# Kernel optimization log

Hardware: AMD Instinct MI355X
Metric: run time of the kernel (lower is better)

The kernel has to match this reference:

```python
import jax, jax.numpy as jnp
import numpy as np

V, D, L, H, DH, F, T, NL = 65536, 1024, 12, 16, 64, 3584, 2048, 2


def _ln(x, w, b):
    m = x.mean(-1, keepdims=True)
    v = ((x - m) ** 2).mean(-1, keepdims=True)
    return (x - m) * jax.lax.rsqrt(v + 1e-5) * w + b


def setup_inputs() -> dict:
    key = jax.random.key(0)
    ks = iter(jax.random.split(key, 64))
    nrm = lambda shape, s=0.02: jax.random.normal(next(ks), shape, jnp.float32) * s
    uni = lambda shape: jax.random.uniform(next(ks), shape, jnp.float32)
    inp = {
        'idx': jax.random.randint(next(ks), (T,), 0, V),
        'emb': nrm((V, D)),
        'ln0_w': jnp.ones((D,), jnp.float32), 'ln0_b': jnp.zeros((D,), jnp.float32),
        'ln1_w': jnp.ones((L, D), jnp.float32), 'ln1_b': jnp.zeros((L, D), jnp.float32),
        'mix_r': uni((L, D)), 'mix_k': uni((L, D)), 'mix_v': uni((L, D)), 'mix_g': uni((L, D)),
        'decay': nrm((L, H, DH), 0.5),  # w = exp(-exp(decay))
        'faaaa': nrm((L, H, DH), 0.1),  # per-head bonus u
        'Wr': nrm((L, D, D)), 'Wk': nrm((L, D, D)), 'Wv': nrm((L, D, D)),
        'Wg': nrm((L, D, D)), 'Wo': nrm((L, D, D)),
        'lnx_w': jnp.ones((L, D), jnp.float32), 'lnx_b': jnp.zeros((L, D), jnp.float32),
        'ln2_w': jnp.ones((L, D), jnp.float32), 'ln2_b': jnp.zeros((L, D), jnp.float32),
        'cmix_k': uni((L, D)), 'cmix_r': uni((L, D)),
        'cWk': nrm((L, D, F)), 'cWv': nrm((L, F, D)), 'cWr': nrm((L, D, D)),
        'lnout_w': jnp.ones((D,), jnp.float32), 'lnout_b': jnp.zeros((D,), jnp.float32),
        'score_w': nrm((NL, D)),
    }
    return inp


def _forward(idx, emb, ln0_w, ln0_b, ln1_w, ln1_b, mix_r, mix_k, mix_v, mix_g,
             decay, faaaa, Wr, Wk, Wv, Wg, Wo, lnx_w, lnx_b, ln2_w, ln2_b,
             cmix_k, cmix_r, cWk, cWv, cWr, lnout_w, lnout_b, score_w):
    x = _ln(emb[idx], ln0_w, ln0_b)  # (T, D); RWKV ln0 on embeddings
    zrow = jnp.zeros((1, D), x.dtype)
    for i in range(L):
        # ---- time mixing (RWKV-5 WKV) ----
        xn = _ln(x, ln1_w[i], ln1_b[i])
        sx = jnp.concatenate([zrow, xn[:-1]], 0)  # token shift, zero init state
        xr = xn * mix_r[i] + sx * (1 - mix_r[i])
        xk = xn * mix_k[i] + sx * (1 - mix_k[i])
        xv = xn * mix_v[i] + sx * (1 - mix_v[i])
        xg = xn * mix_g[i] + sx * (1 - mix_g[i])
        r = (xr @ Wr[i]).reshape(T, H, DH)
        k = (xk @ Wk[i]).reshape(T, H, DH)
        v = (xv @ Wv[i]).reshape(T, H, DH)
        g = jax.nn.silu(xg @ Wg[i])  # (T, D)
        wdec = jnp.exp(-jnp.exp(decay[i]))  # (H, DH) per-channel decay
        uu = faaaa[i]                       # (H, DH) bonus
        def step(S, rkv, wdec=wdec, uu=uu):
            rt, kt, vt = rkv                      # each (H, DH)
            a = kt[:, :, None] * vt[:, None, :]   # (H, DH, DH) outer product
            o = jnp.einsum('hd,hde->he', rt, uu[:, :, None] * a + S)
            return wdec[:, :, None] * S + a, o
        S0 = jnp.zeros((H, DH, DH), x.dtype)
        _, wkv = jax.lax.scan(step, S0, (r, k, v))  # wkv: (T, H, DH)
        # per-head group norm, then affine over full D
        m = wkv.mean(-1, keepdims=True)
        var = ((wkv - m) ** 2).mean(-1, keepdims=True)
        gn = ((wkv - m) * jax.lax.rsqrt(var + 1e-5)).reshape(T, D) * lnx_w[i] + lnx_b[i]
        x = x + (gn * g) @ Wo[i]
        # ---- channel mixing ----
        xn2 = _ln(x, ln2_w[i], ln2_b[i])
        sx2 = jnp.concatenate([zrow, xn2[:-1]], 0)
        xk2 = xn2 * cmix_k[i] + sx2 * (1 - cmix_k[i])
        xr2 = xn2 * cmix_r[i] + sx2 * (1 - cmix_r[i])
        kk = jnp.square(jax.nn.relu(xk2 @ cWk[i]))  # (T, F)
        x = x + jax.nn.sigmoid(xr2 @ cWr[i]) * (kk @ cWv[i])
    x = _ln(x, lnout_w, lnout_b)
    logits = x @ score_w.T  # (T, NL)
    return logits[-1]       # pooled_logits


def reference(idx, emb, ln0_w, ln0_b, ln1_w, ln1_b, mix_r, mix_k, mix_v, mix_g,
              decay, faaaa, Wr, Wk, Wv, Wg, Wo, lnx_w, lnx_b, ln2_w, ln2_b,
              cmix_k, cmix_r, cWk, cWv, cWr, lnout_w, lnout_b, score_w):
    return _forward(idx, emb, ln0_w, ln0_b, ln1_w, ln1_b, mix_r, mix_k, mix_v, mix_g,
                    decay, faaaa, Wr, Wk, Wv, Wg, Wo, lnx_w, lnx_b, ln2_w, ln2_b,
                    cmix_k, cmix_r, cWk, cWv, cWr, lnout_w, lnout_b, score_w)
```

## Files before the change

### kernel.cpp

```cpp
#include <hip/hip_runtime.h>
#include <stdint.h>
#include <math.h>

#define T_SEQ 2048
#define DIM   1024
#define NLAY  12
#define NH    16
#define DHH   64
#define FF    3584
#define CHUNK 32
#define NCH   64

typedef __bf16 bf16;
typedef __attribute__((ext_vector_type(8))) __bf16 bf16x8;
typedef __attribute__((ext_vector_type(4))) __bf16 bf16x4;
typedef __attribute__((ext_vector_type(4))) float f32x4;

#define AS1 __attribute__((address_space(1)))
#define AS3 __attribute__((address_space(3)))

__device__ __forceinline__ void async_cp16(const bf16* g, bf16* l) {
  __builtin_amdgcn_global_load_lds((AS1 void*)(uintptr_t)g, (AS3 void*)l, 16, 0, 0);
}

__device__ __forceinline__ float siluf(float x) { return x / (1.f + expf(-x)); }

__device__ __forceinline__ void block_reduce_4(float& a, float& b, float& c, float& d) {
#pragma unroll
  for (int off = 32; off >= 1; off >>= 1) {
    a += __shfl_xor(a, off, 64);
    b += __shfl_xor(b, off, 64);
    c += __shfl_xor(c, off, 64);
    d += __shfl_xor(d, off, 64);
  }
  __shared__ float red[4][4];
  int wid = threadIdx.x >> 6;
  if ((threadIdx.x & 63) == 0) { red[wid][0] = a; red[wid][1] = b; red[wid][2] = c; red[wid][3] = d; }
  __syncthreads();
  a = red[0][0] + red[1][0] + red[2][0] + red[3][0];
  b = red[0][1] + red[1][1] + red[2][1] + red[3][1];
  c = red[0][2] + red[1][2] + red[2][2] + red[3][2];
  d = red[0][3] + red[1][3] + red[2][3] + red[3][3];
}

__global__ __launch_bounds__(256) void k_embed(const int* __restrict__ idx,
                                               const float* __restrict__ emb,
                                               const float* __restrict__ w,
                                               const float* __restrict__ b,
                                               float* __restrict__ x) {
  int t = blockIdx.x, tid = threadIdx.x, c = tid * 4;
  long row = idx[t];
  float4 xc = *(const float4*)&emb[row * DIM + c];
  float s = xc.x + xc.y + xc.z + xc.w;
  float q = xc.x * xc.x + xc.y * xc.y + xc.z * xc.z + xc.w * xc.w;
  float d2 = 0.f, d3 = 0.f;
  block_reduce_4(s, q, d2, d3);
  float m = s * (1.f / DIM), var = q * (1.f / DIM) - m * m;
  float rs = rsqrtf(var + 1e-5f);
  float4 lw = *(const float4*)&w[c], lb = *(const float4*)&b[c];
  float4 o;
  o.x = (xc.x - m) * rs * lw.x + lb.x;
  o.y = (xc.y - m) * rs * lw.y + lb.y;
  o.z = (xc.z - m) * rs * lw.z + lb.z;
  o.w = (xc.w - m) * rs * lw.w + lb.w;
  *(float4*)&x[(long)t * DIM + c] = o;
}

__global__ __launch_bounds__(256) void k_lnmix(const float* __restrict__ x,
                                               const float* __restrict__ lnw,
                                               const float* __restrict__ lnb,
                                               const float* __restrict__ mx0,
                                               const float* __restrict__ mx1,
                                               const float* __restrict__ mx2,
                                               const float* __restrict__ mx3,
                                               bf16* __restrict__ out, int nmix) {
  int t = blockIdx.x, tid = threadIdx.x, c = tid * 4;
  float4 xc = *(const float4*)&x[(long)t * DIM + c];
  float4 xp = {0.f, 0.f, 0.f, 0.f};
  if (t > 0) xp = *(const float4*)&x[(long)(t - 1) * DIM + c];
  float s1 = xc.x + xc.y + xc.z + xc.w;
  float q1 = xc.x * xc.x + xc.y * xc.y + xc.z * xc.z + xc.w * xc.w;
  float s2 = xp.x + xp.y + xp.z + xp.w;
  float q2 = xp.x * xp.x + xp.y * xp.y + xp.z * xp.z + xp.w * xp.w;
  block_reduce_4(s1, q1, s2, q2);
  float m1 = s1 * (1.f / DIM), v1 = q1 * (1.f / DIM) - m1 * m1, rs1 = rsqrtf(v1 + 1e-5f);
  float m2 = s2 * (1.f / DIM), v2 = q2 * (1.f / DIM) - m2 * m2, rs2 = rsqrtf(v2 + 1e-5f);
  float4 lw = *(const float4*)&lnw[c], lb = *(const float4*)&lnb[c];
  float xs[4] = {xc.x, xc.y, xc.z, xc.w}, xps[4] = {xp.x, xp.y, xp.z, xp.w};
  float lws[4] = {lw.x, lw.y, lw.z, lw.w}, lbs[4] = {lb.x, lb.y, lb.z, lb.w};
  float xn[4], sx[4];
#pragma unroll
  for (int j = 0; j < 4; j++) {
    xn[j] = (xs[j] - m1) * rs1 * lws[j] + lbs[j];
    sx[j] = (t > 0) ? ((xps[j] - m2) * rs2 * lws[j] + lbs[j]) : 0.f;
  }
  for (int mi = 0; mi < nmix; mi++) {
    const float* mp = (mi == 0) ? mx0 : (mi == 1) ? mx1 : (mi == 2) ? mx2 : mx3;
    float4 mv = *(const float4*)&mp[c];
    float ms[4] = {mv.x, mv.y, mv.z, mv.w};
    bf16x4 o;
#pragma unroll
    for (int j = 0; j < 4; j++) o[j] = (bf16)(xn[j] * ms[j] + sx[j] * (1.f - ms[j]));
    *(bf16x4*)&out[(long)mi * T_SEQ * DIM + (long)t * DIM + c] = o;
  }
}

struct TrArgs {
  const float* src[8];
  bf16* dst[8];
  int K[8];
  int N[8];
  int tstart[9];
};

__global__ __launch_bounds__(256) void k_trans(TrArgs a) {
  int bid = blockIdx.x;
  int m = 0;
#pragma unroll
  for (int i = 1; i < 8; i++)
    if (bid >= a.tstart[i]) m = i;
  int tl = bid - a.tstart[m];
  int N = a.N[m], K = a.K[m];
  int ntN = N >> 6;
  int tn = tl % ntN, tk = tl / ntN;
  const float* src = a.src[m];
  bf16* dst = a.dst[m];
  __shared__ __align__(16) float tile[64][65];
  int tid = threadIdx.x;
  int r = tid >> 2, cq = (tid & 3) * 16;
  const float* sp = &src[(long)(tk * 64 + r) * N + tn * 64 + cq];
#pragma unroll
  for (int j = 0; j < 16; j += 4) {
    float4 v = *(const float4*)&sp[j];
    tile[r][cq + j] = v.x;
    tile[r][cq + j + 1] = v.y;
    tile[r][cq + j + 2] = v.z;
    tile[r][cq + j + 3] = v.w;
  }
  __syncthreads();
  int rn = tid >> 2, kq = (tid & 3) * 16;
  bf16* dp = &dst[(long)(tn * 64 + rn) * K + tk * 64 + kq];
#pragma unroll
  for (int h = 0; h < 2; h++) {
    bf16x8 o8;
#pragma unroll
    for (int j = 0; j < 8; j++) o8[j] = (bf16)tile[kq + h * 8 + j][rn];
    *(bf16x8*)&dp[h * 8] = o8;
  }
}

#define BMT 128
#define BKT 32

template <int MODE, int BN>
__global__ __launch_bounds__(256) void k_gemm(const bf16* __restrict__ A,
                                              const bf16* __restrict__ Bt,
                                              void* __restrict__ OUTv,
                                              const float* __restrict__ AUX,
                                              int M, int N, int K,
                                              long zsA, long zsB, long zsO) {
  constexpr int NJ = BN / 32;
  __shared__ __align__(16) bf16 sA[2][BMT * BKT];
  __shared__ __align__(16) bf16 sB[2][BN * BKT];
  int z = blockIdx.z;
  A += (long)z * zsA;
  Bt += (long)z * zsB;
  long zo = (long)z * zsO;
  int n0 = blockIdx.x * BN, m0 = blockIdx.y * BMT;
  int tid = threadIdx.x, lane = tid & 63, wid = tid >> 6;
  int wm = (wid >> 1) * 64, wn = (wid & 1) * (BN / 2);

  f32x4 acc[4][NJ];
#pragma unroll
  for (int i = 0; i < 4; i++)
#pragma unroll
    for (int j = 0; j < NJ; j++) {
      f32x4 zv = {0.f, 0.f, 0.f, 0.f};
      acc[i][j] = zv;
    }

  int r0 = tid >> 2, c0 = (tid & 3) * 8;
  const bf16* gA0 = A + (long)(m0 + r0) * K + c0;
  const bf16* gA1 = A + (long)(m0 + r0 + 64) * K + c0;
  const bf16* gB0 = Bt + (long)(n0 + r0) * K + c0;
  const bf16* gB1 = Bt + (long)(n0 + r0 + 64) * K + c0;

  int kq = (lane >> 4) * 8;
  int fm = lane & 15;

#define STAGE(buf, kk)                                        \
  {                                                           \
    async_cp16(gA0 + (kk), &sA[buf][wid * 512]);              \
    async_cp16(gA1 + (kk), &sA[buf][wid * 512 + 2048]);       \
    async_cp16(gB0 + (kk), &sB[buf][wid * 512]);              \
    if constexpr (BN == 128)                                  \
      async_cp16(gB1 + (kk), &sB[buf][wid * 512 + 2048]);     \
  }

  int nst = K / BKT;
  STAGE(0, 0);
  __syncthreads();

  int cur = 0;
  for (int t = 0; t < nst; ++t) {
    if (t + 1 < nst) STAGE(cur ^ 1, (t + 1) * BKT);
    bf16x8 af[4], bfr[NJ];
#pragma unroll
    for (int i = 0; i < 4; i++)
      af[i] = *(const bf16x8*)&sA[cur][(wm + i * 16 + fm) * BKT + kq];
#pragma unroll
    for (int j = 0; j < NJ; j++)
      bfr[j] = *(const bf16x8*)&sB[cur][(wn + j * 16 + fm) * BKT + kq];
#pragma unroll
    for (int i = 0; i < 4; i++)
#pragma unroll
      for (int j = 0; j < NJ; j++)
        acc[i][j] = __builtin_amdgcn_mfma_f32_16x16x32_bf16(af[i], bfr[j], acc[i][j], 0, 0, 0);
    __syncthreads();
    cur ^= 1;
  }
#undef STAGE

  int col0 = n0 + wn + (lane & 15);
  int row0 = m0 + wm + ((lane >> 4) << 2);
  bf16* Ob = (bf16*)OUTv + zo;
  float* Of = (float*)OUTv + zo;
  bool dosilu = (z == 3);
#pragma unroll
  for (int i = 0; i < 4; i++)
#pragma unroll
    for (int j = 0; j < NJ; j++)
#pragma unroll
      for (int r = 0; r < 4; r++) {
        int row = row0 + i * 16 + r;
        int col = col0 + j * 16;
        long idx = (long)row * N + col;
        float v = acc[i][j][r];
        if constexpr (MODE == 0) {
          if (dosilu) v = siluf(v);
          Ob[idx] = (bf16)v;
        } else if constexpr (MODE == 1) {
          v = fmaxf(v, 0.f);
          Ob[idx] = (bf16)(v * v);
        } else if constexpr (MODE == 2) {
          Of[idx] = 1.f / (1.f + expf(-v));
        } else if constexpr (MODE == 3) {
          Of[idx] += v;
        } else {
          Of[idx] += AUX[idx] * v;
        }
      }
}

__global__ __launch_bounds__(256) void k_wkva(const bf16* __restrict__ kmat,
                                              const bf16* __restrict__ vmat,
                                              const float* __restrict__ decay_l,
                                              float* __restrict__ dS) {
  int c = blockIdx.x, h = blockIdx.y, tid = threadIdx.x;
  __shared__ __align__(16) float kh[CHUNK][DHH];
  __shared__ __align__(16) float vl[CHUNK][DHH];
  int s = tid >> 3, d0 = (tid & 7) * 8;
  float p = (float)(CHUNK - 1 - s);
  long base = (long)(c * CHUNK + s) * DIM + h * DHH + d0;
  bf16x8 k8 = *(const bf16x8*)&kmat[base];
  bf16x8 v8 = *(const bf16x8*)&vmat[base];
#pragma unroll
  for (int j = 0; j < 8; j++) {
    float e2 = expf(decay_l[h * DHH + d0 + j]) * 1.4426950408889634f;
    kh[s][d0 + j] = (float)k8[j] * exp2f(-p * e2);
    vl[s][d0 + j] = (float)v8[j];
  }
  __syncthreads();
  int d = tid >> 2, e0 = (tid & 3) * 16;
  float acc[16];
#pragma unroll
  for (int j = 0; j < 16; j++) acc[j] = 0.f;
  for (int ss = 0; ss < CHUNK; ss++) {
    float kc = kh[ss][d];
#pragma unroll
    for (int j = 0; j < 16; j += 4) {
      float4 vv = *(const float4*)&vl[ss][e0 + j];
      acc[j] = fmaf(kc, vv.x, acc[j]);
      acc[j + 1] = fmaf(kc, vv.y, acc[j + 1]);
      acc[j + 2] = fmaf(kc, vv.z, acc[j + 2]);
      acc[j + 3] = fmaf(kc, vv.w, acc[j + 3]);
    }
  }
  float* out = &dS[(((long)c * NH + h) * DHH + d) * DHH + e0];
#pragma unroll
  for (int j = 0; j < 16; j += 4) {
    float4 o = {acc[j], acc[j + 1], acc[j + 2], acc[j + 3]};
    *(float4*)&out[j] = o;
  }
}

__global__ __launch_bounds__(256) void k_wkvb(float* __restrict__ dS,
                                              const float* __restrict__ decay_l) {
  int id = blockIdx.x * 256 + threadIdx.x;
  int h = id >> 12, d = (id >> 6) & 63;
  float e2 = expf(decay_l[h * DHH + d]);
  float wc = expf(-(float)CHUNK * e2);
  float S = 0.f;
  for (int c = 0; c < NCH; c++) {
    float* p = &dS[(long)c * (NH * DHH * DHH) + id];
    float v = *p;
    *p = S;
    S = wc * S + v;
  }
}

#define WKV_STEP(dd, rc, kc, uc, oa)          \
  {                                           \
    float kv_ = (kc)*ve;                      \
    float tmp_ = fmaf((uc), ve, S[dd]);       \
    oa = fmaf((rc), tmp_, oa);                \
    S[dd] = fmaf(w[dd], S[dd], kv_);          \
  }

__global__ __launch_bounds__(64, 1) void k_wkvc(const bf16* __restrict__ rmat,
                                                const bf16* __restrict__ kmat,
                                                const bf16* __restrict__ vmat,
                                                const bf16* __restrict__ gmat,
                                                const float* __restrict__ decay_l,
                                                const float* __restrict__ faaaa_l,
                                                const float* __restrict__ lnxw,
                                                const float* __restrict__ lnxb,
                                                const float* __restrict__ Sc,
                                                bf16* __restrict__ y) {
  int c = blockIdx.x, h = blockIdx.y, lane = threadIdx.x;
  __shared__ __align__(16) float rl[CHUNK][DHH];
  __shared__ __align__(16) float kl[CHUNK][DHH];
  __shared__ __align__(16) float ukl[CHUNK][DHH];
  __shared__ __align__(16) float vls[CHUNK][DHH];
  __shared__ __align__(16) float wl[DHH];
  float u = faaaa_l[h * DHH + lane];
  wl[lane] = expf(-expf(decay_l[h * DHH + lane]));
  for (int i = 0; i < CHUNK; i++) {
    long base = (long)(c * CHUNK + i) * DIM + h * DHH + lane;
    float rv = (float)rmat[base], kv = (float)kmat[base], vv = (float)vmat[base];
    rl[i][lane] = rv;
    kl[i][lane] = kv;
    ukl[i][lane] = u * kv;
    vls[i][lane] = vv;
  }
  __syncthreads();
  float w[64], S[64];
#pragma unroll
  for (int q = 0; q < 16; q++) {
    float4 t4 = *(const float4*)&wl[q * 4];
    w[q * 4] = t4.x;
    w[q * 4 + 1] = t4.y;
    w[q * 4 + 2] = t4.z;
    w[q * 4 + 3] = t4.w;
  }
  const float* Sp = &Sc[((long)c * NH + h) * DHH * DHH + lane];
#pragma unroll
  for (int d = 0; d < 64; d++) S[d] = Sp[(long)d * DHH];
  float lw = lnxw[h * DHH + lane], lb = lnxb[h * DHH + lane];
#pragma unroll 1
  for (int t = 0; t < CHUNK; t++) {
    float ve = vls[t][lane];
    float o0 = 0.f, o1 = 0.f;
#pragma unroll
    for (int q = 0; q < 16; q++) {
      float4 r4 = *(const float4*)&rl[t][q * 4];
      float4 k4 = *(const float4*)&kl[t][q * 4];
      float4 u4 = *(const float4*)&ukl[t][q * 4];
      WKV_STEP(q * 4 + 0, r4.x, k4.x, u4.x, o0);
      WKV_STEP(q * 4 + 1, r4.y, k4.y, u4.y, o1);
      WKV_STEP(q * 4 + 2, r4.z, k4.z, u4.z, o0);
      WKV_STEP(q * 4 + 3, r4.w, k4.w, u4.w, o1);
    }
    float o = o0 + o1;
    float s1 = o, s2 = o * o;
#pragma unroll
    for (int off = 32; off >= 1; off >>= 1) {
      s1 += __shfl_xor(s1, off, 64);
      s2 += __shfl_xor(s2, off, 64);
    }
    float m = s1 * (1.f / 64.f), var = s2 * (1.f / 64.f) - m * m;
    float gn = (o - m) * rsqrtf(var + 1e-5f) * lw + lb;
    long gi = (long)(c * CHUNK + t) * DIM + h * DHH + lane;
    float gv = (float)gmat[gi];
    y[gi] = (bf16)(gn * gv);
  }
}

__global__ __launch_bounds__(256) void k_final(const float* __restrict__ x,
                                               const float* __restrict__ w,
                                               const float* __restrict__ b,
                                               const float* __restrict__ sw,
                                               float* __restrict__ out) {
  int tid = threadIdx.x, c = tid * 4;
  float4 xc = *(const float4*)&x[(long)(T_SEQ - 1) * DIM + c];
  float s = xc.x + xc.y + xc.z + xc.w;
  float q = xc.x * xc.x + xc.y * xc.y + xc.z * xc.z + xc.w * xc.w;
  float d2 = 0.f, d3 = 0.f;
  block_reduce_4(s, q, d2, d3);
  float m = s * (1.f / DIM), var = q * (1.f / DIM) - m * m;
  float rs = rsqrtf(var + 1e-5f);
  float xs[4] = {xc.x, xc.y, xc.z, xc.w};
  float p0 = 0.f, p1 = 0.f;
#pragma unroll
  for (int j = 0; j < 4; j++) {
    float xn = (xs[j] - m) * rs * w[c + j] + b[c + j];
    p0 += xn * sw[c + j];
    p1 += xn * sw[DIM + c + j];
  }
  float e0 = 0.f, e1 = 0.f;
  block_reduce_4(p0, p1, e0, e1);
  if (tid == 0) {
    out[0] = p0;
    out[1] = p1;
  }
}

extern "C" void kernel_launch(void* const* d_in, const int* in_sizes, int n_in,
                              void* d_out, int out_size, void* d_ws, size_t ws_size,
                              hipStream_t stream) {
  (void)in_sizes; (void)n_in; (void)out_size; (void)ws_size;
  const int* idx = (const int*)d_in[0];
  const float* emb = (const float*)d_in[1];
  const float* ln0w = (const float*)d_in[2];
  const float* ln0b = (const float*)d_in[3];
  const float* ln1w = (const float*)d_in[4];
  const float* ln1b = (const float*)d_in[5];
  const float* mixr = (const float*)d_in[6];
  const float* mixk = (const float*)d_in[7];
  const float* mixv = (const float*)d_in[8];
  const float* mixg = (const float*)d_in[9];
  const float* decay = (const float*)d_in[10];
  const float* faaaa = (const float*)d_in[11];
  const float* Wr = (const float*)d_in[12];
  const float* Wk = (const float*)d_in[13];
  const float* Wv = (const float*)d_in[14];
  const float* Wg = (const float*)d_in[15];
  const float* Wo = (const float*)d_in[16];
  const float* lnxw = (const float*)d_in[17];
  const float* lnxb = (const float*)d_in[18];
  const float* ln2w = (const float*)d_in[19];
  const float* ln2b = (const float*)d_in[20];
  const float* cmixk = (const float*)d_in[21];
  const float* cmixr = (const float*)d_in[22];
  const float* cWk = (const float*)d_in[23];
  const float* cWv = (const float*)d_in[24];
  const float* cWr = (const float*)d_in[25];
  const float* lnoutw = (const float*)d_in[26];
  const float* lnoutb = (const float*)d_in[27];
  const float* scorew = (const float*)d_in[28];

  uint8_t* w8 = (uint8_t*)d_ws;
  float* xbuf = (float*)(w8 + 0);
  bf16* mix4 = (bf16*)(w8 + 8388608);
  bf16* rkvg = (bf16*)(w8 + 25165824);
  bf16* ybuf = (bf16*)(w8 + 41943040);
  float* rrbuf = (float*)(w8 + 46137344);
  bf16* kkbuf = (bf16*)(w8 + 54525952);
  float* dS = (float*)(w8 + 69206016);
  bf16* Wt = (bf16*)(w8 + 85983232);

  const long TD = (long)T_SEQ * DIM;
  const long DD = (long)DIM * DIM;
  const long DF = (long)DIM * FF;

  bf16* WrT = Wt;
  bf16* WoT = Wt + 4 * DD;
  bf16* cWkT = Wt + 5 * DD;
  bf16* cWvT = cWkT + DF;
  bf16* cWrT = cWvT + DF;

  k_embed<<<T_SEQ, 256, 0, stream>>>(idx, emb, ln0w, ln0b, xbuf);

  for (int l = 0; l < NLAY; l++) {
    TrArgs ta;
    ta.src[0] = Wr + (long)l * DD;  ta.dst[0] = Wt + 0 * DD; ta.K[0] = DIM; ta.N[0] = DIM;
    ta.src[1] = Wk + (long)l * DD;  ta.dst[1] = Wt + 1 * DD; ta.K[1] = DIM; ta.N[1] = DIM;
    ta.src[2] = Wv + (long)l * DD;  ta.dst[2] = Wt + 2 * DD; ta.K[2] = DIM; ta.N[2] = DIM;
    ta.src[3] = Wg + (long)l * DD;  ta.dst[3] = Wt + 3 * DD; ta.K[3] = DIM; ta.N[3] = DIM;
    ta.src[4] = Wo + (long)l * DD;  ta.dst[4] = WoT;         ta.K[4] = DIM; ta.N[4] = DIM;
    ta.src[5] = cWk + (long)l * DF; ta.dst[5] = cWkT;        ta.K[5] = DIM; ta.N[5] = FF;
    ta.src[6] = cWv + (long)l * DF; ta.dst[6] = cWvT;        ta.K[6] = FF;  ta.N[6] = DIM;
    ta.src[7] = cWr + (long)l * DD; ta.dst[7] = cWrT;        ta.K[7] = DIM; ta.N[7] = DIM;
    const int ts[9] = {0, 256, 512, 768, 1024, 1280, 2176, 3072, 3328};
    for (int i = 0; i < 9; i++) ta.tstart[i] = ts[i];
    k_trans<<<3328, 256, 0, stream>>>(ta);

    k_lnmix<<<T_SEQ, 256, 0, stream>>>(xbuf, ln1w + l * DIM, ln1b + l * DIM,
                                       mixr + l * DIM, mixk + l * DIM,
                                       mixv + l * DIM, mixg + l * DIM, mix4, 4);

    k_gemm<0, 128><<<dim3(8, 16, 4), 256, 0, stream>>>(mix4, WrT, (void*)rkvg, nullptr,
                                                       T_SEQ, DIM, DIM, TD, DD, TD);

    k_wkva<<<dim3(NCH, NH), 256, 0, stream>>>(rkvg + TD, rkvg + 2 * TD,
                                              decay + (long)l * NH * DHH, dS);
    k_wkvb<<<256, 256, 0, stream>>>(dS, decay + (long)l * NH * DHH);
    k_wkvc<<<dim3(NCH, NH), 64, 0, stream>>>(rkvg, rkvg + TD, rkvg + 2 * TD, rkvg + 3 * TD,
                                             decay + (long)l * NH * DHH,
                                             faaaa + (long)l * NH * DHH,
                                             lnxw + l * DIM, lnxb + l * DIM, dS, ybuf);

    k_gemm<3, 64><<<dim3(16, 16, 1), 256, 0, stream>>>(ybuf, WoT, (void*)xbuf, nullptr,
                                                       T_SEQ, DIM, DIM, 0, 0, 0);

    k_lnmix<<<T_SEQ, 256, 0, stream>>>(xbuf, ln2w + l * DIM, ln2b + l * DIM,
                                       cmixk + l * DIM, cmixr + l * DIM,
                                       nullptr, nullptr, mix4, 2);

    k_gemm<1, 128><<<dim3(28, 16, 1), 256, 0, stream>>>(mix4, cWkT, (void*)kkbuf, nullptr,
                                                        T_SEQ, FF, DIM, 0, 0, 0);
    k_gemm<2, 64><<<dim3(16, 16, 1), 256, 0, stream>>>(mix4 + TD, cWrT, (void*)rrbuf, nullptr,
                                                       T_SEQ, DIM, DIM, 0, 0, 0);
    k_gemm<4, 64><<<dim3(16, 16, 1), 256, 0, stream>>>(kkbuf, cWvT, (void*)xbuf, rrbuf,
                                                       T_SEQ, DIM, FF, 0, 0, 0);
  }

  k_final<<<1, 256, 0, stream>>>(xbuf, lnoutw, lnoutb, scorew, (float*)d_out);
}
```

Before: 3.771 ms.

## Widen GEMM K-tile with LDS swizzle, split-K atomics, and fuse cWk/cWr GEMMs

Doubles the GEMM K tile to 64 and XOR-swizzles the LDS layout to avoid bank conflicts on fragment reads. The Wo and cWv GEMMs, which launch only 256 blocks, are split over two K halves that accumulate into the residual with atomic adds to raise occupancy. The cWk and cWr projections become one launch by laying the transposed weights out contiguously, so a 36-column grid covers both. The trade-offs are non-deterministic float summation order from the atomics and a larger LDS footprint per block.

```diff
diff --git a/kernel.cpp b/kernel.cpp
--- a/kernel.cpp
+++ b/kernel.cpp
@@ -150,9 +150,9 @@
 }
 
 #define BMT 128
-#define BKT 32
-
-template <int MODE, int BN>
+#define BKT 64
+
+template <int MODE, int BN, int KS>
 __global__ __launch_bounds__(256) void k_gemm(const bf16* __restrict__ A,
                                               const bf16* __restrict__ Bt,
                                               void* __restrict__ OUTv,
@@ -160,13 +160,24 @@
                                               int M, int N, int K,
                                               long zsA, long zsB, long zsO) {
   constexpr int NJ = BN / 32;
+  constexpr int NRB = BN / 32;
   __shared__ __align__(16) bf16 sA[2][BMT * BKT];
   __shared__ __align__(16) bf16 sB[2][BN * BKT];
   int z = blockIdx.z;
-  A += (long)z * zsA;
-  Bt += (long)z * zsB;
-  long zo = (long)z * zsO;
+  long zo = 0;
+  long koff = 0;
+  int Klocal = K;
   int n0 = blockIdx.x * BN, m0 = blockIdx.y * BMT;
+  if constexpr (MODE == 0) {
+    A += (long)z * zsA;
+    Bt += (long)z * zsB;
+    zo = (long)z * zsO;
+  } else if constexpr (MODE == 5) {
+    if (n0 >= FF) A += zsA;
+  } else if constexpr (KS > 1) {
+    Klocal = K / KS;
+    koff = (long)z * Klocal;
+  }
   int tid = threadIdx.x, lane = tid & 63, wid = tid >> 6;
   int wm = (wid >> 1) * 64, wn = (wid & 1) * (BN / 2);
 
@@ -179,43 +190,50 @@
       acc[i][j] = zv;
     }
 
-  int r0 = tid >> 2, c0 = (tid & 3) * 8;
-  const bf16* gA0 = A + (long)(m0 + r0) * K + c0;
-  const bf16* gA1 = A + (long)(m0 + r0 + 64) * K + c0;
-  const bf16* gB0 = Bt + (long)(n0 + r0) * K + c0;
-  const bf16* gB1 = Bt + (long)(n0 + r0 + 64) * K + c0;
+  int r0 = tid >> 3;
+  int c0 = ((tid & 7) ^ ((tid >> 3) & 7)) * 8;
+  const bf16* gA0 = A + (long)(m0 + r0) * K + koff + c0;
+  const bf16* gB0 = Bt + (long)(n0 + r0) * K + koff + c0;
+  int ldso = wid * 512;
+
+#define STAGE(buf, kk)                                                          \
+  {                                                                             \
+    _Pragma("unroll")                                                           \
+    for (int rnd = 0; rnd < 4; rnd++)                                           \
+      async_cp16(gA0 + (long)rnd * 32 * K + (kk), &sA[buf][ldso + rnd * 2048]); \
+    _Pragma("unroll")                                                           \
+    for (int rnd = 0; rnd < NRB; rnd++)                                         \
+      async_cp16(gB0 + (long)rnd * 32 * K + (kk), &sB[buf][ldso + rnd * 2048]); \
+  }
 
   int kq = (lane >> 4) * 8;
   int fm = lane & 15;
-
-#define STAGE(buf, kk)                                        \
-  {                                                           \
-    async_cp16(gA0 + (kk), &sA[buf][wid * 512]);              \
-    async_cp16(gA1 + (kk), &sA[buf][wid * 512 + 2048]);       \
-    async_cp16(gB0 + (kk), &sB[buf][wid * 512]);              \
-    if constexpr (BN == 128)                                  \
-      async_cp16(gB1 + (kk), &sB[buf][wid * 512 + 2048]);     \
-  }
-
-  int nst = K / BKT;
+  int nst = Klocal / BKT;
   STAGE(0, 0);
   __syncthreads();
 
   int cur = 0;
   for (int t = 0; t < nst; ++t) {
     if (t + 1 < nst) STAGE(cur ^ 1, (t + 1) * BKT);
-    bf16x8 af[4], bfr[NJ];
-#pragma unroll
-    for (int i = 0; i < 4; i++)
-      af[i] = *(const bf16x8*)&sA[cur][(wm + i * 16 + fm) * BKT + kq];
-#pragma unroll
-    for (int j = 0; j < NJ; j++)
-      bfr[j] = *(const bf16x8*)&sB[cur][(wn + j * 16 + fm) * BKT + kq];
-#pragma unroll
-    for (int i = 0; i < 4; i++)
-#pragma unroll
-      for (int j = 0; j < NJ; j++)
-        acc[i][j] = __builtin_amdgcn_mfma_f32_16x16x32_bf16(af[i], bfr[j], acc[i][j], 0, 0, 0);
+#pragma unroll
+    for (int kk2 = 0; kk2 < 2; kk2++) {
+      bf16x8 af[4], bfr[NJ];
+#pragma unroll
+      for (int i = 0; i < 4; i++) {
+        int row = wm + i * 16 + fm;
+        af[i] = *(const bf16x8*)&sA[cur][row * BKT + ((kk2 * 32 + kq) ^ ((row & 7) << 3))];
+      }
+#pragma unroll
+      for (int j = 0; j < NJ; j++) {
+        int row = wn + j * 16 + fm;
+        bfr[j] = *(const bf16x8*)&sB[cur][row * BKT + ((kk2 * 32 + kq) ^ ((row & 7) << 3))];
+      }
+#pragma unroll
+      for (int i = 0; i < 4; i++)
+#pragma unroll
+        for (int j = 0; j < NJ; j++)
+          acc[i][j] = __builtin_amdgcn_mfma_f32_16x16x32_bf16(af[i], bfr[j], acc[i][j], 0, 0, 0);
+    }
     __syncthreads();
     cur ^= 1;
   }
@@ -239,15 +257,19 @@
         if constexpr (MODE == 0) {
           if (dosilu) v = siluf(v);
           Ob[idx] = (bf16)v;
-        } else if constexpr (MODE == 1) {
-          v = fmaxf(v, 0.f);
-          Ob[idx] = (bf16)(v * v);
-        } else if constexpr (MODE == 2) {
-          Of[idx] = 1.f / (1.f + expf(-v));
         } else if constexpr (MODE == 3) {
-          Of[idx] += v;
+          if constexpr (KS > 1) unsafeAtomicAdd(&Of[idx], v);
+          else Of[idx] += v;
+        } else if constexpr (MODE == 4) {
+          if constexpr (KS > 1) unsafeAtomicAdd(&Of[idx], AUX[idx] * v);
+          else Of[idx] += AUX[idx] * v;
         } else {
-          Of[idx] += AUX[idx] * v;
+          if (n0 < FF) {
+            float vr = fmaxf(v, 0.f);
+            ((bf16*)OUTv)[(long)row * FF + col] = (bf16)(vr * vr);
+          } else {
+            ((float*)AUX)[(long)row * DIM + (col - FF)] = 1.f / (1.f + expf(-v));
+          }
         }
       }
 }
@@ -466,8 +488,8 @@
   bf16* WrT = Wt;
   bf16* WoT = Wt + 4 * DD;
   bf16* cWkT = Wt + 5 * DD;
-  bf16* cWvT = cWkT + DF;
-  bf16* cWrT = cWvT + DF;
+  bf16* cWrT = cWkT + DF;
+  bf16* cWvT = cWrT + DD;
 
   k_embed<<<T_SEQ, 256, 0, stream>>>(idx, emb, ln0w, ln0b, xbuf);
 
@@ -479,9 +501,9 @@
     ta.src[3] = Wg + (long)l * DD;  ta.dst[3] = Wt + 3 * DD; ta.K[3] = DIM; ta.N[3] = DIM;
     ta.src[4] = Wo + (long)l * DD;  ta.dst[4] = WoT;         ta.K[4] = DIM; ta.N[4] = DIM;
     ta.src[5] = cWk + (long)l * DF; ta.dst[5] = cWkT;        ta.K[5] = DIM; ta.N[5] = FF;
-    ta.src[6] = cWv + (long)l * DF; ta.dst[6] = cWvT;        ta.K[6] = FF;  ta.N[6] = DIM;
-    ta.src[7] = cWr + (long)l * DD; ta.dst[7] = cWrT;        ta.K[7] = DIM; ta.N[7] = DIM;
-    const int ts[9] = {0, 256, 512, 768, 1024, 1280, 2176, 3072, 3328};
+    ta.src[6] = cWr + (long)l * DD; ta.dst[6] = cWrT;        ta.K[6] = DIM; ta.N[6] = DIM;
+    ta.src[7] = cWv + (long)l * DF; ta.dst[7] = cWvT;        ta.K[7] = FF;  ta.N[7] = DIM;
+    const int ts[9] = {0, 256, 512, 768, 1024, 1280, 2176, 2432, 3328};
     for (int i = 0; i < 9; i++) ta.tstart[i] = ts[i];
     k_trans<<<3328, 256, 0, stream>>>(ta);
 
@@ -489,8 +511,8 @@
                                        mixr + l * DIM, mixk + l * DIM,
                                        mixv + l * DIM, mixg + l * DIM, mix4, 4);
 
-    k_gemm<0, 128><<<dim3(8, 16, 4), 256, 0, stream>>>(mix4, WrT, (void*)rkvg, nullptr,
-                                                       T_SEQ, DIM, DIM, TD, DD, TD);
+    k_gemm<0, 128, 1><<<dim3(8, 16, 4), 256, 0, stream>>>(mix4, WrT, (void*)rkvg, nullptr,
+                                                          T_SEQ, DIM, DIM, TD, DD, TD);
 
     k_wkva<<<dim3(NCH, NH), 256, 0, stream>>>(rkvg + TD, rkvg + 2 * TD,
                                               decay + (long)l * NH * DHH, dS);
@@ -500,19 +522,19 @@
                                              faaaa + (long)l * NH * DHH,
                                              lnxw + l * DIM, lnxb + l * DIM, dS, ybuf);
 
-    k_gemm<3, 64><<<dim3(16, 16, 1), 256, 0, stream>>>(ybuf, WoT, (void*)xbuf, nullptr,
-                                                       T_SEQ, DIM, DIM, 0, 0, 0);
+    k_gemm<3, 64, 2><<<dim3(16, 16, 2), 256, 0, stream>>>(ybuf, WoT, (void*)xbuf, nullptr,
+                                                          T_SEQ, DIM, DIM, 0, 0, 0);
 
     k_lnmix<<<T_SEQ, 256, 0, stream>>>(xbuf, ln2w + l * DIM, ln2b + l * DIM,
                                        cmixk + l * DIM, cmixr + l * DIM,
                                        nullptr, nullptr, mix4, 2);
 
-    k_gemm<1, 128><<<dim3(28, 16, 1), 256, 0, stream>>>(mix4, cWkT, (void*)kkbuf, nullptr,
-                                                        T_SEQ, FF, DIM, 0, 0, 0);
-    k_gemm<2, 64><<<dim3(16, 16, 1), 256, 0, stream>>>(mix4 + TD, cWrT, (void*)rrbuf, nullptr,
-                                                       T_SEQ, DIM, DIM, 0, 0, 0);
-    k_gemm<4, 64><<<dim3(16, 16, 1), 256, 0, stream>>>(kkbuf, cWvT, (void*)xbuf, rrbuf,
-                                                       T_SEQ, DIM, FF, 0, 0, 0);
+    k_gemm<5, 128, 1><<<dim3(36, 16, 1), 256, 0, stream>>>(mix4, cWkT, (void*)kkbuf,
+                                                           (const float*)rrbuf,
+                                                           T_SEQ, FF, DIM, TD, 0, 0);
+
+    k_gemm<4, 64, 2><<<dim3(16, 16, 2), 256, 0, stream>>>(kkbuf, cWvT, (void*)xbuf, rrbuf,
+                                                          T_SEQ, DIM, FF, 0, 0, 0);
   }
 
   k_final<<<1, 256, 0, stream>>>(xbuf, lnoutw, lnoutb, scorew, (float*)d_out);
```

New measurement: 3.367 ms. 10.7% less time.
